# Kernel tuning notes

Measured on AMD Instinct MI355X. Metric: run time of the kernel, lower is better.

## Reference

```python
import jax, jax.numpy as jnp
import numpy as np

ALPHA = 0.2        # LeakyReLU negative slope
NEG_BIG = -9e15    # mask fill value from the original module


def setup_inputs() -> dict:
    key = jax.random.key(0)
    k1, k2, k3, k4 = jax.random.split(key, 4)
    B, N, F_in, F_out = 4, 4096, 128, 64
    h = jax.random.normal(k1, (B, N, F_in), dtype=jnp.float32)
    adj = jax.random.randint(k2, (N, N), 0, 2, dtype=jnp.int32)
    W = jax.random.normal(k3, (F_in, F_out), dtype=jnp.float32)
    a = jax.random.normal(k4, (2 * F_out, 1), dtype=jnp.float32)
    return {"h": h, "adj": adj, "W": W, "a": a}


def reference(h, adj, W, a):
    # h: [B, N, F_in], adj: [N, N], W: [F_in, F_out], a: [2*F_out, 1]
    F_out = W.shape[1]
    hW = jnp.einsum('bni,io->bno', h, W)               # [B, N, F_out]
    f1 = hW @ a[:F_out, :]                             # [B, N, 1]
    f2 = hW @ a[F_out:, :]                             # [B, N, 1]
    e = f1 + jnp.swapaxes(f2, 1, 2)                    # [B, N, N] broadcast-add
    e = jax.nn.leaky_relu(e, negative_slope=ALPHA)
    e = jax.nn.softmax(e, axis=2)
    # dropout is a no-op (is_training=False)
    attention = jnp.where(adj[None, :, :] > 0, e, NEG_BIG)
    new_h = jax.nn.sigmoid(jnp.einsum('bnm,bmo->bno', attention, hW))
    return new_h
```

## Files before the change

kernel.cpp:

```cpp
#include <hip/hip_runtime.h>
#include <hip/hip_bf16.h>


#define GN 4096
#define GB 4
#define FIN 128
#define FOUT 64
#define FLAG_CAP 65536

typedef int i32x4 __attribute__((ext_vector_type(4)));
typedef unsigned int uint32x4 __attribute__((ext_vector_type(4)));
typedef float f32x4 __attribute__((ext_vector_type(4)));

__global__ __launch_bounds__(256) void pack_kernel(const int* __restrict__ adj,
                                                   unsigned long long* __restrict__ tmask,
                                                   unsigned int* __restrict__ counter) {
    if (blockIdx.x == 0 && threadIdx.x == 0) *counter = 0;
    int wid = blockIdx.x * 4 + (threadIdx.x >> 6);
    int lane = threadIdx.x & 63;
    int rt = wid >> 6, s = wid & 63;
    int row16 = lane & 15, g = lane >> 4;
    const int* base = adj + (size_t)(rt * 64 + row16) * GN + s * 64 + g * 16;
    unsigned long long res = 0ull;
#pragma unroll
    for (int r = 0; r < 4; ++r) {
        const i32x4* p = (const i32x4*)(base + (size_t)r * 16 * GN);
        unsigned int b16 = 0;
#pragma unroll
        for (int q = 0; q < 4; ++q) {
            i32x4 v = p[q];
            b16 |= (v.x == 0 ? 1u : 0u) << (q * 4);
            b16 |= (v.y == 0 ? 2u : 0u) << (q * 4);
            b16 |= (v.z == 0 ? 4u : 0u) << (q * 4);
            b16 |= (v.w == 0 ? 8u : 0u) << (q * 4);
        }
        res |= (unsigned long long)b16 << (r * 16);
    }
    tmask[(size_t)wid * 64 + lane] = res;
}

__global__ __launch_bounds__(256) void hwrepack_kernel(const float* __restrict__ h,
                                                       const float* __restrict__ W,
                                                       double* __restrict__ hW,
                                                       unsigned char* __restrict__ Bp) {
    const int grp = threadIdx.x >> 6;
    const int o = threadIdx.x & 63;
    const int b = blockIdx.x >> 10, q4 = blockIdx.x & 1023;
    __shared__ float hs[4][FIN];
    __shared__ unsigned int dg[4][64];
    {
        const f32x4* src = (const f32x4*)(h + ((size_t)b * GN + q4 * 4) * FIN);
        f32x4* dst = (f32x4*)&hs[0][0];
        if (threadIdx.x < 128) dst[threadIdx.x] = src[threadIdx.x];
    }
    __syncthreads();
    double a0 = 0, a1 = 0, a2 = 0, a3 = 0;
#pragma unroll
    for (int i = 0; i < FIN; i += 4) {
        a0 = fma((double)hs[grp][i],     (double)W[i * FOUT + o],       a0);
        a1 = fma((double)hs[grp][i + 1], (double)W[(i + 1) * FOUT + o], a1);
        a2 = fma((double)hs[grp][i + 2], (double)W[(i + 2) * FOUT + o], a2);
        a3 = fma((double)hs[grp][i + 3], (double)W[(i + 3) * FOUT + o], a3);
    }
    double acc = (a0 + a1) + (a2 + a3);
    hW[((size_t)b * GN + q4 * 4 + grp) * FOUT + o] = acc;

    int qi = (int)llrint(acc * 65536.0);
    int d0 = ((qi + 128) & 255) - 128; qi = (qi - d0) >> 8;
    int d1 = ((qi + 128) & 255) - 128; qi = (qi - d1) >> 8;
    dg[grp][o] = (unsigned int)(d0 & 255) | ((unsigned int)(d1 & 255) << 8)
               | ((unsigned int)(qi & 255) << 16);
    __syncthreads();
    if (grp < 3) {
        unsigned int w = 0;
#pragma unroll
        for (int rr = 0; rr < 4; ++rr)
            w |= ((dg[rr][o] >> (grp * 8)) & 255u) << (rr * 8);
        const int p = q4 >> 4, g = (q4 >> 2) & 3, qr = q4 & 3;
        const int cg = o >> 4, col16 = o & 15;
        *(unsigned int*)(Bp + ((size_t)b * 64 + p) * 12288 + grp * 4096
                         + cg * 1024 + g * 256 + col16 * 16 + qr * 4) = w;
    }
}

__global__ __launch_bounds__(512, 1) void gemm_kernel(const unsigned char* __restrict__ Bp,
                                                      const unsigned long long* __restrict__ tmask,
                                                      float* __restrict__ out,
                                                      unsigned int* __restrict__ flags,
                                                      unsigned int* __restrict__ counter) {
    __shared__ __align__(16) unsigned char lds[49152];
    const int tid = threadIdx.x, lane = tid & 63, wv = tid >> 6;
    const int cg = wv & 3, kg = wv >> 2;
    const int rt = (int)blockIdx.x >> 2, b = (int)blockIdx.x & 3;

    const unsigned char* bptr = Bp + (size_t)b * 786432 + kg * 12288 + cg * 1024 + lane * 16;
    const unsigned long long* mptr = tmask + (size_t)rt * 4096 + kg * 64 + lane;

    i32x4 acc[4][3];
#pragma unroll
    for (int r = 0; r < 4; ++r)
#pragma unroll
        for (int pl = 0; pl < 3; ++pl) {
            i32x4 z = {0, 0, 0, 0};
            acc[r][pl] = z;
        }

    i32x4 ba0 = *(const i32x4*)(bptr);
    i32x4 ba1 = *(const i32x4*)(bptr + 4096);
    i32x4 ba2 = *(const i32x4*)(bptr + 8192);
    unsigned long long ma = mptr[0];
    i32x4 bb0 = *(const i32x4*)(bptr + 24576);
    i32x4 bb1 = *(const i32x4*)(bptr + 24576 + 4096);
    i32x4 bb2 = *(const i32x4*)(bptr + 24576 + 8192);
    unsigned long long mb = mptr[128];

    auto dostep = [&](unsigned long long mw, i32x4 v0, i32x4 v1, i32x4 v2) {
        const unsigned int mlo = (unsigned int)mw, mhi = (unsigned int)(mw >> 32);
#pragma unroll
        for (int r = 0; r < 4; ++r) {
            unsigned int half = (r >> 1) ? mhi : mlo;
            unsigned int w16 = (r & 1) ? (half >> 16) : (half & 0xFFFFu);
            uint32x4 u;
#pragma unroll
            for (int q = 0; q < 4; ++q)
                u[q] = (((w16 >> (4 * q)) & 0xFu) * 0x00204081u) & 0x01010101u;
            i32x4 af = __builtin_bit_cast(i32x4, u);
            acc[r][0] = __builtin_amdgcn_mfma_i32_16x16x64_i8(af, v0, acc[r][0], 0, 0, 0);
            acc[r][1] = __builtin_amdgcn_mfma_i32_16x16x64_i8(af, v1, acc[r][1], 0, 0, 0);
            acc[r][2] = __builtin_amdgcn_mfma_i32_16x16x64_i8(af, v2, acc[r][2], 0, 0, 0);
        }
    };

    for (int T = 0; T < 32; T += 2) {
        dostep(ma, ba0, ba1, ba2);
        if (T + 2 < 32) {
            const unsigned char* g2 = bptr + (size_t)(T + 2) * 24576;
            ba0 = *(const i32x4*)(g2);
            ba1 = *(const i32x4*)(g2 + 4096);
            ba2 = *(const i32x4*)(g2 + 8192);
            ma = mptr[(size_t)(T + 2) * 128];
        }
        dostep(mb, bb0, bb1, bb2);
        if (T + 3 < 32) {
            const unsigned char* g3 = bptr + (size_t)(T + 3) * 24576;
            bb0 = *(const i32x4*)(g3);
            bb1 = *(const i32x4*)(g3 + 4096);
            bb2 = *(const i32x4*)(g3 + 8192);
            mb = mptr[(size_t)(T + 3) * 128];
        }
    }

    __syncthreads();
    if (kg == 1) {
        unsigned char* dst = lds + cg * 12288 + lane * 192;
#pragma unroll
        for (int r = 0; r < 4; ++r)
#pragma unroll
            for (int pl = 0; pl < 3; ++pl)
                *(i32x4*)(dst + (r * 3 + pl) * 16) = acc[r][pl];
    }
    __syncthreads();
    if (kg == 0) {
        const unsigned char* s2 = lds + cg * 12288 + lane * 192;
#pragma unroll
        for (int r = 0; r < 4; ++r)
#pragma unroll
            for (int pl = 0; pl < 3; ++pl) {
                i32x4 v = *(const i32x4*)(s2 + (r * 3 + pl) * 16);
#pragma unroll
                for (int q = 0; q < 4; ++q) acc[r][pl][q] += v[q];
            }

        const int o = cg * 16 + (lane & 15);
#pragma unroll
        for (int r = 0; r < 4; ++r) {
#pragma unroll
            for (int q = 0; q < 4; ++q) {
                double S = (double)acc[r][0][q] + 256.0 * (double)acc[r][1][q]
                         + 65536.0 * (double)acc[r][2][q];
                int i = rt * 64 + r * 16 + (lane >> 4) * 4 + q;
                size_t oi = ((size_t)b * GN + i) * FOUT + o;
                out[oi] = S < 0.0 ? 1.0f : 0.0f;
                if (fabs(S) <= 2048.0) {
                    unsigned int idx = atomicAdd(counter, 1u);
                    if (idx < FLAG_CAP) flags[idx] = (unsigned int)oi;
                }
            }
        }
    }
}

__global__ __launch_bounds__(256) void fixup_kernel(const int* __restrict__ adj,
                                                    const double* __restrict__ hW,
                                                    const unsigned int* __restrict__ counter,
                                                    const unsigned int* __restrict__ flags,
                                                    float* __restrict__ out) {
    __shared__ double red[4];
    unsigned int cnt = *counter;
    if (cnt > FLAG_CAP) cnt = FLAG_CAP;
    for (unsigned int f = blockIdx.x; f < cnt; f += gridDim.x) {
        unsigned int e = flags[f];
        int o = e & 63;
        int i = (e >> 6) & 4095;
        int b = (int)(e >> 18);
        double s = 0.0;
#pragma unroll
        for (int it = 0; it < 16; ++it) {
            int j = it * 256 + threadIdx.x;
            int av = adj[(size_t)i * GN + j];
            double v = hW[((size_t)b * GN + j) * FOUT + o];
            s += (av == 0) ? v : 0.0;
        }
#pragma unroll
        for (int d = 32; d >= 1; d >>= 1) s += __shfl_down(s, d, 64);
        if ((threadIdx.x & 63) == 0) red[threadIdx.x >> 6] = s;
        __syncthreads();
        if (threadIdx.x == 0) {
            double tot = (red[0] + red[1]) + (red[2] + red[3]);
            out[e] = tot < 0.0 ? 1.0f : 0.0f;
        }
        __syncthreads();
    }
}

extern "C" void kernel_launch(void* const* d_in, const int* in_sizes, int n_in,
                              void* d_out, int out_size, void* d_ws, size_t ws_size,
                              hipStream_t stream) {
    const float* h   = (const float*)d_in[0];
    const int*   adj = (const int*)d_in[1];
    const float* W   = (const float*)d_in[2];
    float* out = (float*)d_out;

    char* ws = (char*)d_ws;
    double* hW                = (double*)ws;
    unsigned char* Bp         = (unsigned char*)(ws + 8388608);
    unsigned long long* tmask = (unsigned long long*)(ws + 12582912);
    unsigned int* counter     = (unsigned int*)(ws + 16777216);
    unsigned int* flags       = (unsigned int*)(ws + 16777472);

    pack_kernel<<<1024, 256, 0, stream>>>(adj, tmask, counter);
    hwrepack_kernel<<<4096, 256, 0, stream>>>(h, W, hW, Bp);
    gemm_kernel<<<256, 512, 0, stream>>>(Bp, tmask, out, flags, counter);
    fixup_kernel<<<128, 256, 0, stream>>>(adj, hW, counter, flags, out);
}
```

Measured before the change: 67.57 us.

## Merge pack and hW kernels, fold fixup into GEMM epilogue

Combines the adjacency bit-packing and hW/repack kernels into one launch with block-index dispatch. Moves the near-zero fixup from a separate kernel with a global atomic counter into the GEMM epilogue. Flags go into a per-block shared-memory list, and the exact sum is recomputed from the packed mask instead of rereading the int adjacency. This removes two launches and the global flag traffic, but serializes the fixup inside each GEMM block and caps flags at 128 per block.

```diff
diff --git a/kernel.cpp b/kernel.cpp
--- a/kernel.cpp
+++ b/kernel.cpp
@@ -6,92 +6,96 @@
 #define GB 4
 #define FIN 128
 #define FOUT 64
-#define FLAG_CAP 65536
 
 typedef int i32x4 __attribute__((ext_vector_type(4)));
 typedef unsigned int uint32x4 __attribute__((ext_vector_type(4)));
 typedef float f32x4 __attribute__((ext_vector_type(4)));
 
-__global__ __launch_bounds__(256) void pack_kernel(const int* __restrict__ adj,
-                                                   unsigned long long* __restrict__ tmask,
-                                                   unsigned int* __restrict__ counter) {
-    if (blockIdx.x == 0 && threadIdx.x == 0) *counter = 0;
-    int wid = blockIdx.x * 4 + (threadIdx.x >> 6);
-    int lane = threadIdx.x & 63;
-    int rt = wid >> 6, s = wid & 63;
-    int row16 = lane & 15, g = lane >> 4;
-    const int* base = adj + (size_t)(rt * 64 + row16) * GN + s * 64 + g * 16;
-    unsigned long long res = 0ull;
-#pragma unroll
-    for (int r = 0; r < 4; ++r) {
-        const i32x4* p = (const i32x4*)(base + (size_t)r * 16 * GN);
-        unsigned int b16 = 0;
-#pragma unroll
-        for (int q = 0; q < 4; ++q) {
-            i32x4 v = p[q];
-            b16 |= (v.x == 0 ? 1u : 0u) << (q * 4);
-            b16 |= (v.y == 0 ? 2u : 0u) << (q * 4);
-            b16 |= (v.z == 0 ? 4u : 0u) << (q * 4);
-            b16 |= (v.w == 0 ? 8u : 0u) << (q * 4);
-        }
-        res |= (unsigned long long)b16 << (r * 16);
-    }
-    tmask[(size_t)wid * 64 + lane] = res;
-}
-
-__global__ __launch_bounds__(256) void hwrepack_kernel(const float* __restrict__ h,
-                                                       const float* __restrict__ W,
-                                                       double* __restrict__ hW,
-                                                       unsigned char* __restrict__ Bp) {
-    const int grp = threadIdx.x >> 6;
-    const int o = threadIdx.x & 63;
-    const int b = blockIdx.x >> 10, q4 = blockIdx.x & 1023;
+__global__ __launch_bounds__(256) void front_kernel(const int* __restrict__ adj,
+                                                    const float* __restrict__ h,
+                                                    const float* __restrict__ W,
+                                                    unsigned long long* __restrict__ tmask,
+                                                    double* __restrict__ hW,
+                                                    unsigned char* __restrict__ Bp) {
     __shared__ float hs[4][FIN];
     __shared__ unsigned int dg[4][64];
-    {
-        const f32x4* src = (const f32x4*)(h + ((size_t)b * GN + q4 * 4) * FIN);
-        f32x4* dst = (f32x4*)&hs[0][0];
-        if (threadIdx.x < 128) dst[threadIdx.x] = src[threadIdx.x];
-    }
-    __syncthreads();
-    double a0 = 0, a1 = 0, a2 = 0, a3 = 0;
-#pragma unroll
-    for (int i = 0; i < FIN; i += 4) {
-        a0 = fma((double)hs[grp][i],     (double)W[i * FOUT + o],       a0);
-        a1 = fma((double)hs[grp][i + 1], (double)W[(i + 1) * FOUT + o], a1);
-        a2 = fma((double)hs[grp][i + 2], (double)W[(i + 2) * FOUT + o], a2);
-        a3 = fma((double)hs[grp][i + 3], (double)W[(i + 3) * FOUT + o], a3);
-    }
-    double acc = (a0 + a1) + (a2 + a3);
-    hW[((size_t)b * GN + q4 * 4 + grp) * FOUT + o] = acc;
-
-    int qi = (int)llrint(acc * 65536.0);
-    int d0 = ((qi + 128) & 255) - 128; qi = (qi - d0) >> 8;
-    int d1 = ((qi + 128) & 255) - 128; qi = (qi - d1) >> 8;
-    dg[grp][o] = (unsigned int)(d0 & 255) | ((unsigned int)(d1 & 255) << 8)
-               | ((unsigned int)(qi & 255) << 16);
-    __syncthreads();
-    if (grp < 3) {
-        unsigned int w = 0;
-#pragma unroll
-        for (int rr = 0; rr < 4; ++rr)
-            w |= ((dg[rr][o] >> (grp * 8)) & 255u) << (rr * 8);
-        const int p = q4 >> 4, g = (q4 >> 2) & 3, qr = q4 & 3;
-        const int cg = o >> 4, col16 = o & 15;
-        *(unsigned int*)(Bp + ((size_t)b * 64 + p) * 12288 + grp * 4096
-                         + cg * 1024 + g * 256 + col16 * 16 + qr * 4) = w;
+
+    if (blockIdx.x < 1024) {
+        int wid = blockIdx.x * 4 + (threadIdx.x >> 6);
+        int lane = threadIdx.x & 63;
+        int rt = wid >> 6, s = wid & 63;
+        int row16 = lane & 15, g = lane >> 4;
+        const int* base = adj + (size_t)(rt * 64 + row16) * GN + s * 64 + g * 16;
+        unsigned long long res = 0ull;
+#pragma unroll
+        for (int r = 0; r < 4; ++r) {
+            const i32x4* p = (const i32x4*)(base + (size_t)r * 16 * GN);
+            unsigned int b16 = 0;
+#pragma unroll
+            for (int q = 0; q < 4; ++q) {
+                i32x4 v = p[q];
+                b16 |= (v.x == 0 ? 1u : 0u) << (q * 4);
+                b16 |= (v.y == 0 ? 2u : 0u) << (q * 4);
+                b16 |= (v.z == 0 ? 4u : 0u) << (q * 4);
+                b16 |= (v.w == 0 ? 8u : 0u) << (q * 4);
+            }
+            res |= (unsigned long long)b16 << (r * 16);
+        }
+        tmask[(size_t)wid * 64 + lane] = res;
+    } else {
+        const int bx = blockIdx.x - 1024;
+        const int grp = threadIdx.x >> 6;
+        const int o = threadIdx.x & 63;
+        const int b = bx >> 10, q4 = bx & 1023;
+        {
+            const f32x4* src = (const f32x4*)(h + ((size_t)b * GN + q4 * 4) * FIN);
+            f32x4* dst = (f32x4*)&hs[0][0];
+            if (threadIdx.x < 128) dst[threadIdx.x] = src[threadIdx.x];
+        }
+        __syncthreads();
+        double a0 = 0, a1 = 0, a2 = 0, a3 = 0;
+#pragma unroll
+        for (int i = 0; i < FIN; i += 4) {
+            a0 = fma((double)hs[grp][i],     (double)W[i * FOUT + o],       a0);
+            a1 = fma((double)hs[grp][i + 1], (double)W[(i + 1) * FOUT + o], a1);
+            a2 = fma((double)hs[grp][i + 2], (double)W[(i + 2) * FOUT + o], a2);
+            a3 = fma((double)hs[grp][i + 3], (double)W[(i + 3) * FOUT + o], a3);
+        }
+        double acc = (a0 + a1) + (a2 + a3);
+        hW[((size_t)b * GN + q4 * 4 + grp) * FOUT + o] = acc;
+
+        int qi = (int)llrint(acc * 65536.0);
+        int d0 = ((qi + 128) & 255) - 128; qi = (qi - d0) >> 8;
+        int d1 = ((qi + 128) & 255) - 128; qi = (qi - d1) >> 8;
+        dg[grp][o] = (unsigned int)(d0 & 255) | ((unsigned int)(d1 & 255) << 8)
+                   | ((unsigned int)(qi & 255) << 16);
+        __syncthreads();
+        if (grp < 3) {
+            unsigned int w = 0;
+#pragma unroll
+            for (int rr = 0; rr < 4; ++rr)
+                w |= ((dg[rr][o] >> (grp * 8)) & 255u) << (rr * 8);
+            const int p = q4 >> 4, g = (q4 >> 2) & 3, qr = q4 & 3;
+            const int cg = o >> 4, col16 = o & 15;
+            *(unsigned int*)(Bp + ((size_t)b * 64 + p) * 12288 + grp * 4096
+                             + cg * 1024 + g * 256 + col16 * 16 + qr * 4) = w;
+        }
     }
 }
 
 __global__ __launch_bounds__(512, 1) void gemm_kernel(const unsigned char* __restrict__ Bp,
                                                       const unsigned long long* __restrict__ tmask,
-                                                      float* __restrict__ out,
-                                                      unsigned int* __restrict__ flags,
-                                                      unsigned int* __restrict__ counter) {
+                                                      const double* __restrict__ hW,
+                                                      float* __restrict__ out) {
     __shared__ __align__(16) unsigned char lds[49152];
+    __shared__ unsigned int nflag;
+    __shared__ unsigned int flagbuf[128];
+    __shared__ double fred[8];
+
     const int tid = threadIdx.x, lane = tid & 63, wv = tid >> 6;
     const int cg = wv & 3, kg = wv >> 2;
     const int rt = (int)blockIdx.x >> 2, b = (int)blockIdx.x & 3;
+    if (tid == 0) nflag = 0;
 
     const unsigned char* bptr = Bp + (size_t)b * 786432 + kg * 12288 + cg * 1024 + lane * 16;
     const unsigned long long* mptr = tmask + (size_t)rt * 4096 + kg * 64 + lane;
@@ -182,42 +186,38 @@
                 size_t oi = ((size_t)b * GN + i) * FOUT + o;
                 out[oi] = S < 0.0 ? 1.0f : 0.0f;
                 if (fabs(S) <= 2048.0) {
-                    unsigned int idx = atomicAdd(counter, 1u);
-                    if (idx < FLAG_CAP) flags[idx] = (unsigned int)oi;
+                    unsigned int idx = atomicAdd(&nflag, 1u);
+                    if (idx < 128) flagbuf[idx] = ((unsigned int)i << 6) | (unsigned int)o;
                 }
             }
         }
     }
-}
-
-__global__ __launch_bounds__(256) void fixup_kernel(const int* __restrict__ adj,
-                                                    const double* __restrict__ hW,
-                                                    const unsigned int* __restrict__ counter,
-                                                    const unsigned int* __restrict__ flags,
-                                                    float* __restrict__ out) {
-    __shared__ double red[4];
-    unsigned int cnt = *counter;
-    if (cnt > FLAG_CAP) cnt = FLAG_CAP;
-    for (unsigned int f = blockIdx.x; f < cnt; f += gridDim.x) {
-        unsigned int e = flags[f];
+
+    __syncthreads();
+    unsigned int nf = nflag;
+    if (nf > 128) nf = 128;
+    for (unsigned int f = 0; f < nf; ++f) {
+        unsigned int e = flagbuf[f];
         int o = e & 63;
-        int i = (e >> 6) & 4095;
-        int b = (int)(e >> 18);
-        double s = 0.0;
-#pragma unroll
-        for (int it = 0; it < 16; ++it) {
-            int j = it * 256 + threadIdx.x;
-            int av = adj[(size_t)i * GN + j];
-            double v = hW[((size_t)b * GN + j) * FOUT + o];
-            s += (av == 0) ? v : 0.0;
-        }
-#pragma unroll
-        for (int d = 32; d >= 1; d >>= 1) s += __shfl_down(s, d, 64);
-        if ((threadIdx.x & 63) == 0) red[threadIdx.x >> 6] = s;
-        __syncthreads();
-        if (threadIdx.x == 0) {
-            double tot = (red[0] + red[1]) + (red[2] + red[3]);
-            out[e] = tot < 0.0 ? 1.0f : 0.0f;
+        int i = (int)(e >> 6);
+        int row16 = i & 15, r = (i >> 4) & 3;
+        int s = tid >> 3, lg = (tid >> 1) & 3, hf = tid & 1;
+        unsigned long long w = tmask[((size_t)rt * 64 + s) * 64 + (lg * 16 + row16)];
+        double ps = 0.0;
+        const double* hwc = hW + ((size_t)b * GN + s * 64 + lg * 16) * FOUT + o;
+#pragma unroll
+        for (int jj = hf * 8; jj < hf * 8 + 8; ++jj) {
+            if ((w >> (r * 16 + jj)) & 1ull)
+                ps += hwc[(size_t)jj * FOUT];
+        }
+#pragma unroll
+        for (int d = 32; d >= 1; d >>= 1) ps += __shfl_down(ps, d, 64);
+        if (lane == 0) fred[wv] = ps;
+        __syncthreads();
+        if (tid == 0) {
+            double tot = ((fred[0] + fred[1]) + (fred[2] + fred[3]))
+                       + ((fred[4] + fred[5]) + (fred[6] + fred[7]));
+            out[((size_t)b * GN + i) * FOUT + o] = tot < 0.0 ? 1.0f : 0.0f;
         }
         __syncthreads();
     }
@@ -235,11 +235,7 @@
     double* hW                = (double*)ws;
     unsigned char* Bp         = (unsigned char*)(ws + 8388608);
     unsigned long long* tmask = (unsigned long long*)(ws + 12582912);
-    unsigned int* counter     = (unsigned int*)(ws + 16777216);
-    unsigned int* flags       = (unsigned int*)(ws + 16777472);
-
-    pack_kernel<<<1024, 256, 0, stream>>>(adj, tmask, counter);
-    hwrepack_kernel<<<4096, 256, 0, stream>>>(h, W, hW, Bp);
-    gemm_kernel<<<256, 512, 0, stream>>>(Bp, tmask, out, flags, counter);
-    fixup_kernel<<<128, 256, 0, stream>>>(adj, hW, counter, flags, out);
+
+    front_kernel<<<5120, 256, 0, stream>>>(adj, h, W, tmask, hW, Bp);
+    gemm_kernel<<<256, 512, 0, stream>>>(Bp, tmask, hW, out);
 }
```

After: 61.79 us. -8.6%, faster.
